# Kernel tuning notes

Hardware: AMD Instinct MI355X
Metric: run time of the kernel (lower is better)

## Reference

```python
import jax, jax.numpy as jnp
import numpy as np

# Module hyperparameters (from init_kwargs)
KH, KW = 3, 3          # kernel_size (must be 3x3: code hardcodes center tap 4 and 9 search positions)
SH, SW = 1, 1          # stride
PH, PW = 4, 4          # padding
DH, DW = 4, 4          # dilation
SD = DH // 2           # search_dilation


def setup_inputs() -> dict:
    key = jax.random.key(0)
    # positive depth values in meters-like range
    depth = jax.random.uniform(key, (4, 1, 480, 640), dtype=jnp.float32) * 10.0
    return {"depth": depth}


def _offset_search(depth):
    b, _, h, w = depth.shape
    outH = (h + 2 * PH - DH * (KH - 1) - 1) // SH + 1
    outW = (w + 2 * PW - DW * (KW - 1) - 1) // SW + 1
    d = depth[:, 0]  # [b, h, w]

    # --- first unfold: 3x3 window, dilation=SD, padding=SD, stride=1 ---
    # 9 zero-padded shifted copies of the depth map (the search samples)
    dp = jnp.pad(d, ((0, 0), (SD, SD), (SD, SD)))
    S = jnp.stack([dp[:, SD * r: SD * r + h, SD * c: SD * c + w]
                   for r in range(3) for c in range(3)], axis=1)  # [b, 9, h, w]

    # --- second unfold: kernel 3x3, dilation=(DH,DW), padding=(PH,PW), stride=(SH,SW) ---
    Sp = jnp.pad(S, ((0, 0), (0, 0), (PH, PH), (PW, PW)))
    rspan = SH * (outH - 1) + 1
    cspan = SW * (outW - 1) + 1
    taps = [Sp[:, :, DH * r: DH * r + rspan: SH, DW * c: DW * c + cspan: SW]
            for r in range(KH) for c in range(KW)]
    sample = jnp.stack(taps, axis=2)  # [b, 9(search), 9(kernel), outH, outW]

    # --- center tap (index 4) of unfold(depth) ---
    dpp = jnp.pad(d, ((0, 0), (PH, PH), (PW, PW)))
    center = dpp[:, DH: DH + rspan: SH, DW: DW + cspan: SW]  # [b, outH, outW]

    sample = jnp.abs(sample - center[:, None, None])

    # mask invalid search positions with +inf for border kernel taps 1,3,5,7
    inf = jnp.float32(jnp.inf)
    row_idx = jnp.array([0, 1, 2, 6, 7, 8])
    col_idx = jnp.array([0, 2, 3, 5, 6, 8])
    sample = sample.at[:, col_idx, 1].set(inf)
    sample = sample.at[:, row_idx, 3].set(inf)
    sample = sample.at[:, row_idx, 5].set(inf)
    sample = sample.at[:, col_idx, 7].set(inf)

    # argmin over the 9 search positions (first occurrence, like torch.min)
    idx = jnp.argmin(sample, axis=1)          # [b, 9, outH, outW]
    off_h = (idx // KH - 1) * SD
    off_w = (idx % KW - 1) * SD
    return jnp.concatenate([off_h, off_w], axis=1).astype(jnp.int32)  # [b, 18, outH, outW]


def reference(depth):
    return _offset_search(depth)
```

## Files before the change

kernel.cpp:

```cpp
#include <hip/hip_runtime.h>


#define BATCH 4
#define IH 480
#define IW 640

__global__ __launch_bounds__(256) void depth_offset_kernel(
    const float* __restrict__ d, int* __restrict__ out) {
  int idx = blockIdx.x * blockDim.x + threadIdx.x;
  if (idx >= BATCH * IH * IW) return;
  int ox = idx % IW;
  int t = idx / IW;
  int oy = t % IH;
  int b = t / IH;

  const float* __restrict__ db = d + (size_t)b * (IH * IW);
  float center = db[oy * IW + ox];

  float nb[7][7];
#pragma unroll
  for (int i = 0; i < 7; ++i) {
    int y = oy + 2 * i - 6;
    bool yok = ((unsigned)y < (unsigned)IH);
#pragma unroll
    for (int jj = 0; jj < 7; ++jj) {
      int x = ox + 2 * jj - 6;
      float v = 0.0f;
      if (yok && ((unsigned)x < (unsigned)IW)) v = db[y * IW + x];
      nb[i][jj] = v;
    }
  }

  const size_t plane = (size_t)IH * IW;
  int* __restrict__ outb = out + (size_t)b * 18 * plane;
  size_t pix = (size_t)oy * IW + ox;

#pragma unroll
  for (int j = 0; j < 9; ++j) {
    const int jr = j / 3, jc = j % 3;
    int Y = oy + 4 * (jr - 1);
    int X = ox + 4 * (jc - 1);
    bool jok = ((unsigned)Y < (unsigned)IH) && ((unsigned)X < (unsigned)IW);

    float best = __builtin_huge_valf();
    int bk = 0;
#pragma unroll
    for (int k = 0; k < 9; ++k) {
      const int kr = k / 3, kc = k % 3;
      bool allowed = true;
      if (j == 1 || j == 7) allowed = (kc == 1);
      if (j == 3 || j == 5) allowed = (kr == 1);
      if (!allowed) continue;

      float v = jok ? nb[2 * jr + kr][2 * jc + kc] : 0.0f;
      float diff = fabsf(v - center);
      if (diff < best) {
        best = diff;
        bk = k;
      }
    }
    outb[(size_t)j * plane + pix] = (bk / 3 - 1) * 2;
    outb[(size_t)(9 + j) * plane + pix] = (bk % 3 - 1) * 2;
  }
}

extern "C" void kernel_launch(void* const* d_in, const int* in_sizes, int n_in,
                              void* d_out, int out_size, void* d_ws, size_t ws_size,
                              hipStream_t stream) {
  const float* depth = (const float*)d_in[0];
  int* out = (int*)d_out;
  const int total = BATCH * IH * IW;
  const int block = 256;
  const int grid = (total + block - 1) / block;
  depth_offset_kernel<<<grid, block, 0, stream>>>(depth, out);
}
```

Baseline: 99.00 us.

## Pre-pad depth into workspace and process four pixels per thread with vector I/O

Result: slower. 102.3 us (+3.4%).

```diff
diff --git a/kernel.cpp b/kernel.cpp
--- a/kernel.cpp
+++ b/kernel.cpp
@@ -4,8 +4,174 @@
 #define BATCH 4
 #define IH 480
 #define IW 640
-
-__global__ __launch_bounds__(256) void depth_offset_kernel(
+#define PPW 656
+#define PPH 492
+#define PADBYTES ((size_t)BATCH * PPH * PPW * 4)
+
+__global__ __launch_bounds__(256) void pad_kernel(const float* __restrict__ d,
+                                                  float* __restrict__ pd) {
+  int idx = blockIdx.x * blockDim.x + threadIdx.x;
+  const int n4 = BATCH * PPH * (PPW / 4);
+  if (idx >= n4) return;
+  int c4 = idx % (PPW / 4);
+  int t = idx / (PPW / 4);
+  int r = t % PPH;
+  int b = t / PPH;
+  int y = r - 6;
+  float4 v = make_float4(0.f, 0.f, 0.f, 0.f);
+  if ((unsigned)y < (unsigned)IH) {
+    const float* src = d + ((size_t)b * IH + y) * IW;
+    int xb = c4 * 4 - 6;
+    float* vp = (float*)&v;
+#pragma unroll
+    for (int q = 0; q < 4; ++q) {
+      int x = xb + q;
+      if ((unsigned)x < (unsigned)IW) vp[q] = src[x];
+    }
+  }
+  ((float4*)pd)[idx] = v;
+}
+
+__global__ __launch_bounds__(256) void depth_offset_main(
+    const float* __restrict__ pd, int* __restrict__ out) {
+  const int NG = IW / 4;
+  int g = blockIdx.x * blockDim.x + threadIdx.x;
+  if (g >= BATCH * IH * NG) return;
+  int gx = g % NG;
+  int t = g / NG;
+  int oy = t % IH;
+  int b = t / IH;
+  int x0 = gx * 4;
+
+  const float* base = pd + ((size_t)b * PPH + oy) * PPW + x0;
+
+  float r0[16], r1[16], r2[16], r3[16], r4[16], r5[16], r6[16];
+#define LDROW(arr, i)                                              \
+  {                                                                \
+    const float4* rp = (const float4*)(base + (size_t)(2 * (i)) * PPW); \
+    *(float4*)&arr[0] = rp[0];                                     \
+    *(float4*)&arr[4] = rp[1];                                     \
+    *(float4*)&arr[8] = rp[2];                                     \
+    *(float4*)&arr[12] = rp[3];                                    \
+  }
+
+  const size_t plane = (size_t)IH * IW;
+  int* obase = out + (size_t)b * 18 * plane + (size_t)oy * IW + x0;
+#define STORE2(J, oh, ow)                                          \
+  {                                                                \
+    *(int4*)(obase + (size_t)(J)*plane) =                          \
+        make_int4(oh[0], oh[1], oh[2], oh[3]);                     \
+    *(int4*)(obase + (size_t)(9 + (J)) * plane) =                  \
+        make_int4(ow[0], ow[1], ow[2], ow[3]);                     \
+  }
+
+  bool yok0 = (oy >= 4), yok2 = (oy <= IH - 5);
+  bool xokL[4], xokR[4];
+#pragma unroll
+  for (int p = 0; p < 4; ++p) {
+    xokL[p] = (x0 + p >= 4);
+    xokR[p] = (x0 + p <= IW - 5);
+  }
+
+#define CAND(val, H, W)                  \
+  {                                      \
+    float df = fabsf((val)-cc);          \
+    if (df < best) {                     \
+      best = df;                         \
+      bh = (H);                          \
+      bw = (W);                          \
+    }                                    \
+  }
+
+#define DO_TAP9(J, RA, RB, RC, JC4, OKEXPR, FH, FW)                 \
+  {                                                                 \
+    int oh[4], ow[4];                                               \
+    _Pragma("unroll") for (int p = 0; p < 4; ++p) {                 \
+      float cc = cen[p];                                            \
+      int cb = p + (JC4);                                           \
+      float best = fabsf(RA[cb] - cc);                              \
+      int bh = -2, bw = -2;                                         \
+      CAND(RA[cb + 2], -2, 0)                                       \
+      CAND(RA[cb + 4], -2, 2)                                       \
+      CAND(RB[cb], 0, -2)                                           \
+      CAND(RB[cb + 2], 0, 0)                                        \
+      CAND(RB[cb + 4], 0, 2)                                        \
+      CAND(RC[cb], 2, -2)                                           \
+      CAND(RC[cb + 2], 2, 0)                                        \
+      CAND(RC[cb + 4], 2, 2)                                        \
+      bool ok = (OKEXPR);                                           \
+      oh[p] = ok ? bh : (FH);                                       \
+      ow[p] = ok ? bw : (FW);                                       \
+    }                                                               \
+    STORE2(J, oh, ow)                                               \
+  }
+
+#define DO_TAPV(J, RA, RB, RC, OKEXPR)                              \
+  {                                                                 \
+    int oh[4], ow[4];                                               \
+    _Pragma("unroll") for (int p = 0; p < 4; ++p) {                 \
+      float cc = cen[p];                                            \
+      int cb = p + 6;                                               \
+      float best = fabsf(RA[cb] - cc);                              \
+      int bh = -2;                                                  \
+      {                                                             \
+        float df = fabsf(RB[cb] - cc);                              \
+        if (df < best) { best = df; bh = 0; }                       \
+      }                                                             \
+      {                                                             \
+        float df = fabsf(RC[cb] - cc);                              \
+        if (df < best) { best = df; bh = 2; }                       \
+      }                                                             \
+      bool ok = (OKEXPR);                                           \
+      oh[p] = ok ? bh : -2;                                         \
+      ow[p] = 0;                                                    \
+    }                                                               \
+    STORE2(J, oh, ow)                                               \
+  }
+
+#define DO_TAPH(J, R, JC4, OKEXPR)                                  \
+  {                                                                 \
+    int oh[4], ow[4];                                               \
+    _Pragma("unroll") for (int p = 0; p < 4; ++p) {                 \
+      float cc = cen[p];                                            \
+      int cb = p + (JC4);                                           \
+      float best = fabsf(R[cb] - cc);                               \
+      int bw = -2;                                                  \
+      {                                                             \
+        float df = fabsf(R[cb + 2] - cc);                           \
+        if (df < best) { best = df; bw = 0; }                       \
+      }                                                             \
+      {                                                             \
+        float df = fabsf(R[cb + 4] - cc);                           \
+        if (df < best) { best = df; bw = 2; }                       \
+      }                                                             \
+      bool ok = (OKEXPR);                                           \
+      oh[p] = 0;                                                    \
+      ow[p] = ok ? bw : -2;                                         \
+    }                                                               \
+    STORE2(J, oh, ow)                                               \
+  }
+
+  LDROW(r0, 0)
+  LDROW(r1, 1)
+  LDROW(r2, 2)
+  LDROW(r3, 3)
+  float cen[4] = {r3[6], r3[7], r3[8], r3[9]};
+  LDROW(r4, 4)
+  DO_TAP9(0, r0, r1, r2, 0, yok0 && xokL[p], -2, -2)
+  DO_TAPV(1, r0, r1, r2, yok0)
+  DO_TAP9(2, r0, r1, r2, 8, yok0 && xokR[p], -2, -2)
+  LDROW(r5, 5)
+  LDROW(r6, 6)
+  DO_TAPH(3, r3, 0, xokL[p])
+  DO_TAP9(4, r2, r3, r4, 4, true, 0, 0)
+  DO_TAPH(5, r3, 8, xokR[p])
+  DO_TAP9(6, r4, r5, r6, 0, yok2 && xokL[p], -2, -2)
+  DO_TAPV(7, r4, r5, r6, yok2)
+  DO_TAP9(8, r4, r5, r6, 8, yok2 && xokR[p], -2, -2)
+}
+
+__global__ __launch_bounds__(256) void depth_offset_fallback(
     const float* __restrict__ d, int* __restrict__ out) {
   int idx = blockIdx.x * blockDim.x + threadIdx.x;
   if (idx >= BATCH * IH * IW) return;
@@ -13,10 +179,8 @@
   int t = idx / IW;
   int oy = t % IH;
   int b = t / IH;
-
-  const float* __restrict__ db = d + (size_t)b * (IH * IW);
+  const float* db = d + (size_t)b * (IH * IW);
   float center = db[oy * IW + ox];
-
   float nb[7][7];
 #pragma unroll
   for (int i = 0; i < 7; ++i) {
@@ -30,18 +194,15 @@
       nb[i][jj] = v;
     }
   }
-
   const size_t plane = (size_t)IH * IW;
-  int* __restrict__ outb = out + (size_t)b * 18 * plane;
+  int* outb = out + (size_t)b * 18 * plane;
   size_t pix = (size_t)oy * IW + ox;
-
 #pragma unroll
   for (int j = 0; j < 9; ++j) {
     const int jr = j / 3, jc = j % 3;
     int Y = oy + 4 * (jr - 1);
     int X = ox + 4 * (jc - 1);
     bool jok = ((unsigned)Y < (unsigned)IH) && ((unsigned)X < (unsigned)IW);
-
     float best = __builtin_huge_valf();
     int bk = 0;
 #pragma unroll
@@ -51,7 +212,6 @@
       if (j == 1 || j == 7) allowed = (kc == 1);
       if (j == 3 || j == 5) allowed = (kr == 1);
       if (!allowed) continue;
-
       float v = jok ? nb[2 * jr + kr][2 * jc + kc] : 0.0f;
       float diff = fabsf(v - center);
       if (diff < best) {
@@ -69,8 +229,14 @@
                               hipStream_t stream) {
   const float* depth = (const float*)d_in[0];
   int* out = (int*)d_out;
-  const int total = BATCH * IH * IW;
-  const int block = 256;
-  const int grid = (total + block - 1) / block;
-  depth_offset_kernel<<<grid, block, 0, stream>>>(depth, out);
-}
+  if (ws_size >= PADBYTES) {
+    float* pd = (float*)d_ws;
+    const int n4 = BATCH * PPH * (PPW / 4);
+    pad_kernel<<<(n4 + 255) / 256, 256, 0, stream>>>(depth, pd);
+    const int ngroups = BATCH * IH * (IW / 4);
+    depth_offset_main<<<(ngroups + 255) / 256, 256, 0, stream>>>(pd, out);
+  } else {
+    const int total = BATCH * IH * IW;
+    depth_offset_fallback<<<(total + 255) / 256, 256, 0, stream>>>(depth, out);
+  }
+}
```

## Tile depth into shared memory and compute four pixels per thread

Applied to the files above, without the earlier changes.

After: 104.7 us. 1.06x slower.

```diff
diff --git a/kernel.cpp b/kernel.cpp
--- a/kernel.cpp
+++ b/kernel.cpp
@@ -4,64 +4,192 @@
 #define BATCH 4
 #define IH 480
 #define IW 640
+#define TW 128
+#define TH 8
+#define LW 144
+#define LH 20
+#define NXT (IW / TW)
+#define NYT (IH / TH)
+
+typedef int iv4 __attribute__((ext_vector_type(4)));
 
 __global__ __launch_bounds__(256) void depth_offset_kernel(
     const float* __restrict__ d, int* __restrict__ out) {
-  int idx = blockIdx.x * blockDim.x + threadIdx.x;
-  if (idx >= BATCH * IH * IW) return;
-  int ox = idx % IW;
-  int t = idx / IW;
-  int oy = t % IH;
-  int b = t / IH;
+  __shared__ float T[LH * LW];
+
+  int blk = blockIdx.x;
+  int xt = blk % NXT;
+  int t = blk / NXT;
+  int yt = t % NYT;
+  int b = t / NYT;
+  int x0 = xt * TW;
+  int oy0 = yt * TH;
 
   const float* __restrict__ db = d + (size_t)b * (IH * IW);
-  float center = db[oy * IW + ox];
-
-  float nb[7][7];
+
+  bool interior = (xt > 0) && (xt < NXT - 1) && (yt > 0) && (yt < NYT - 1);
+  if (interior) {
+    const float* src = db + (size_t)(oy0 - 6) * IW + (x0 - 8);
 #pragma unroll
-  for (int i = 0; i < 7; ++i) {
-    int y = oy + 2 * i - 6;
-    bool yok = ((unsigned)y < (unsigned)IH);
-#pragma unroll
-    for (int jj = 0; jj < 7; ++jj) {
-      int x = ox + 2 * jj - 6;
-      float v = 0.0f;
-      if (yok && ((unsigned)x < (unsigned)IW)) v = db[y * IW + x];
-      nb[i][jj] = v;
-    }
-  }
-
-  const size_t plane = (size_t)IH * IW;
-  int* __restrict__ outb = out + (size_t)b * 18 * plane;
-  size_t pix = (size_t)oy * IW + ox;
-
-#pragma unroll
-  for (int j = 0; j < 9; ++j) {
-    const int jr = j / 3, jc = j % 3;
-    int Y = oy + 4 * (jr - 1);
-    int X = ox + 4 * (jc - 1);
-    bool jok = ((unsigned)Y < (unsigned)IH) && ((unsigned)X < (unsigned)IW);
-
-    float best = __builtin_huge_valf();
-    int bk = 0;
-#pragma unroll
-    for (int k = 0; k < 9; ++k) {
-      const int kr = k / 3, kc = k % 3;
-      bool allowed = true;
-      if (j == 1 || j == 7) allowed = (kc == 1);
-      if (j == 3 || j == 5) allowed = (kr == 1);
-      if (!allowed) continue;
-
-      float v = jok ? nb[2 * jr + kr][2 * jc + kc] : 0.0f;
-      float diff = fabsf(v - center);
-      if (diff < best) {
-        best = diff;
-        bk = k;
+    for (int it = 0; it < 3; ++it) {
+      int i = threadIdx.x + it * 256;
+      if (i < LH * (LW / 4)) {
+        int r = i / (LW / 4);
+        int c4 = i % (LW / 4);
+        *(float4*)&T[r * LW + c4 * 4] =
+            *(const float4*)(src + (size_t)r * IW + c4 * 4);
       }
     }
-    outb[(size_t)j * plane + pix] = (bk / 3 - 1) * 2;
-    outb[(size_t)(9 + j) * plane + pix] = (bk % 3 - 1) * 2;
-  }
+  } else {
+#pragma unroll
+    for (int it = 0; it < 12; ++it) {
+      int i = threadIdx.x + it * 256;
+      if (i < LH * LW) {
+        int r = i / LW;
+        int c = i % LW;
+        int y = oy0 + r - 6;
+        int x = x0 + c - 8;
+        float v = 0.0f;
+        if (((unsigned)y < (unsigned)IH) && ((unsigned)x < (unsigned)IW))
+          v = db[(size_t)y * IW + x];
+        T[r * LW + c] = v;
+      }
+    }
+  }
+  __syncthreads();
+
+  int gxi = threadIdx.x & 31;
+  int ry = threadIdx.x >> 5;
+  int px = x0 + gxi * 4;
+  int oy = oy0 + ry;
+
+  float R0[20], R1[20], R2[20];
+#define LDW(R, TROW)                                             \
+  {                                                              \
+    const float4* rp = (const float4*)&T[(TROW) * LW + gxi * 4]; \
+    *(float4*)&R[0] = rp[0];                                     \
+    *(float4*)&R[4] = rp[1];                                     \
+    *(float4*)&R[8] = rp[2];                                     \
+    *(float4*)&R[12] = rp[3];                                    \
+    *(float4*)&R[16] = rp[4];                                    \
+  }
+
+  float4 cen4 = *(const float4*)&T[(ry + 6) * LW + gxi * 4 + 8];
+  float cen[4] = {cen4.x, cen4.y, cen4.z, cen4.w};
+
+  const size_t plane = (size_t)IH * IW;
+  int* obase = out + (size_t)b * 18 * plane + (size_t)oy * IW + px;
+#define STORE2(J, oh, ow)                                              \
+  {                                                                    \
+    iv4 vh = {oh[0], oh[1], oh[2], oh[3]};                             \
+    iv4 vw = {ow[0], ow[1], ow[2], ow[3]};                             \
+    __builtin_nontemporal_store(vh, (iv4*)(obase + (size_t)(J)*plane)); \
+    __builtin_nontemporal_store(vw, (iv4*)(obase + (size_t)(9 + (J)) * plane)); \
+  }
+
+  bool yok0 = (oy >= 4), yok2 = (oy <= IH - 5);
+  bool xokL[4], xokR[4];
+#pragma unroll
+  for (int p = 0; p < 4; ++p) {
+    xokL[p] = (px + p >= 4);
+    xokR[p] = (px + p <= IW - 5);
+  }
+
+#define CAND(val, H, W)         \
+  {                             \
+    float df = fabsf((val)-cc); \
+    if (df < best) {            \
+      best = df;                \
+      bh = (H);                 \
+      bw = (W);                 \
+    }                           \
+  }
+
+#define DO_TAP9(J, RA, RB, RC, CB0, OKP, FH, FW)    \
+  {                                                 \
+    int oh[4], ow[4];                               \
+    _Pragma("unroll") for (int p = 0; p < 4; ++p) { \
+      float cc = cen[p];                            \
+      int cb = p + (CB0);                           \
+      float best = fabsf(RA[cb] - cc);              \
+      int bh = -2, bw = -2;                         \
+      CAND(RA[cb + 2], -2, 0)                       \
+      CAND(RA[cb + 4], -2, 2)                       \
+      CAND(RB[cb], 0, -2)                           \
+      CAND(RB[cb + 2], 0, 0)                        \
+      CAND(RB[cb + 4], 0, 2)                        \
+      CAND(RC[cb], 2, -2)                           \
+      CAND(RC[cb + 2], 2, 0)                        \
+      CAND(RC[cb + 4], 2, 2)                        \
+      bool ok = (OKP);                              \
+      oh[p] = ok ? bh : (FH);                       \
+      ow[p] = ok ? bw : (FW);                       \
+    }                                               \
+    STORE2(J, oh, ow)                               \
+  }
+
+#define DO_TAPV(J, RA, RB, RC, OKE)                 \
+  {                                                 \
+    int oh[4], ow[4];                               \
+    _Pragma("unroll") for (int p = 0; p < 4; ++p) { \
+      float cc = cen[p];                            \
+      int cb = p + 8;                               \
+      float best = fabsf(RA[cb] - cc);              \
+      int bh = -2;                                  \
+      {                                             \
+        float df = fabsf(RB[cb] - cc);              \
+        if (df < best) { best = df; bh = 0; }       \
+      }                                             \
+      {                                             \
+        float df = fabsf(RC[cb] - cc);              \
+        if (df < best) { best = df; bh = 2; }       \
+      }                                             \
+      bool ok = (OKE);                              \
+      oh[p] = ok ? bh : -2;                         \
+      ow[p] = 0;                                    \
+    }                                               \
+    STORE2(J, oh, ow)                               \
+  }
+
+#define DO_TAPH(J, R, CB0, OKP)                     \
+  {                                                 \
+    int oh[4], ow[4];                               \
+    _Pragma("unroll") for (int p = 0; p < 4; ++p) { \
+      float cc = cen[p];                            \
+      int cb = p + (CB0);                           \
+      float best = fabsf(R[cb] - cc);               \
+      int bw = -2;                                  \
+      {                                             \
+        float df = fabsf(R[cb + 2] - cc);           \
+        if (df < best) { best = df; bw = 0; }       \
+      }                                             \
+      {                                             \
+        float df = fabsf(R[cb + 4] - cc);           \
+        if (df < best) { best = df; bw = 2; }       \
+      }                                             \
+      bool ok = (OKP);                              \
+      oh[p] = 0;                                    \
+      ow[p] = ok ? bw : -2;                         \
+    }                                               \
+    STORE2(J, oh, ow)                               \
+  }
+
+  LDW(R0, ry)
+  LDW(R1, ry + 2)
+  LDW(R2, ry + 4)
+  DO_TAP9(0, R0, R1, R2, 2, yok0 && xokL[p], -2, -2)
+  DO_TAPV(1, R0, R1, R2, yok0)
+  DO_TAP9(2, R0, R1, R2, 10, yok0 && xokR[p], -2, -2)
+  LDW(R0, ry + 6)
+  LDW(R1, ry + 8)
+  DO_TAPH(3, R0, 2, xokL[p])
+  DO_TAP9(4, R2, R0, R1, 6, true, 0, 0)
+  DO_TAPH(5, R0, 10, xokR[p])
+  LDW(R2, ry + 10)
+  LDW(R0, ry + 12)
+  DO_TAP9(6, R1, R2, R0, 2, yok2 && xokL[p], -2, -2)
+  DO_TAPV(7, R1, R2, R0, yok2)
+  DO_TAP9(8, R1, R2, R0, 10, yok2 && xokR[p], -2, -2)
 }
 
 extern "C" void kernel_launch(void* const* d_in, const int* in_sizes, int n_in,
@@ -69,8 +197,6 @@
                               hipStream_t stream) {
   const float* depth = (const float*)d_in[0];
   int* out = (int*)d_out;
-  const int total = BATCH * IH * IW;
-  const int block = 256;
-  const int grid = (total + block - 1) / block;
-  depth_offset_kernel<<<grid, block, 0, stream>>>(depth, out);
+  const int nblocks = BATCH * NYT * NXT;
+  depth_offset_kernel<<<nblocks, 256, 0, stream>>>(depth, out);
 }
```

## Process four pixels per thread with vectorized row loads and nontemporal vector stores

Applied to the files above, without the earlier changes.

New measurement: 103.4 us. +4.5%, slower.

```diff
diff --git a/kernel.cpp b/kernel.cpp
--- a/kernel.cpp
+++ b/kernel.cpp
@@ -4,64 +4,173 @@
 #define BATCH 4
 #define IH 480
 #define IW 640
+#define NG (IW / 4)
+#define NPIX ((long)BATCH * IH * IW)
 
-__global__ __launch_bounds__(256) void depth_offset_kernel(
+typedef int iv4 __attribute__((ext_vector_type(4)));
+typedef float fv4 __attribute__((ext_vector_type(4)));
+
+__global__ __launch_bounds__(64) void depth_offset_kernel(
     const float* __restrict__ d, int* __restrict__ out) {
-  int idx = blockIdx.x * blockDim.x + threadIdx.x;
-  if (idx >= BATCH * IH * IW) return;
-  int ox = idx % IW;
-  int t = idx / IW;
+  int g = blockIdx.x * 64 + threadIdx.x;
+  int gx = g % NG;
+  int t = g / NG;
   int oy = t % IH;
   int b = t / IH;
+  int px = gx * 4;
 
   const float* __restrict__ db = d + (size_t)b * (IH * IW);
-  float center = db[oy * IW + ox];
 
-  float nb[7][7];
-#pragma unroll
-  for (int i = 0; i < 7; ++i) {
-    int y = oy + 2 * i - 6;
-    bool yok = ((unsigned)y < (unsigned)IH);
-#pragma unroll
-    for (int jj = 0; jj < 7; ++jj) {
-      int x = ox + 2 * jj - 6;
-      float v = 0.0f;
-      if (yok && ((unsigned)x < (unsigned)IW)) v = db[y * IW + x];
-      nb[i][jj] = v;
-    }
+  fv4 cen4 = *(const fv4*)(db + (size_t)oy * IW + px);
+  float cen[4] = {cen4.x, cen4.y, cen4.z, cen4.w};
+
+  bool xsafe = (px >= 8) && (px <= IW - 12);
+
+  float R0[20], R1[20], R2[20];
+#define LDG(R, i)                                                        \
+  {                                                                      \
+    int y = oy + 2 * (i) - 6;                                            \
+    if ((unsigned)y < (unsigned)IH) {                                    \
+      long a = ((long)(b * IH + y)) * IW + px - 8;                       \
+      if (xsafe || (a >= 0 && a + 20 <= NPIX)) {                         \
+        const fv4* rp = (const fv4*)(d + a);                             \
+        *(fv4*)&R[0] = rp[0];                                            \
+        *(fv4*)&R[4] = rp[1];                                            \
+        *(fv4*)&R[8] = rp[2];                                            \
+        *(fv4*)&R[12] = rp[3];                                           \
+        *(fv4*)&R[16] = rp[4];                                           \
+        if (!xsafe) {                                                    \
+          _Pragma("unroll") for (int c = 0; c < 20; ++c) {               \
+            int x = px + c - 8;                                          \
+            if ((unsigned)x >= (unsigned)IW) R[c] = 0.f;                 \
+          }                                                              \
+        }                                                                \
+      } else {                                                           \
+        const float* ry_ = db + (size_t)y * IW;                          \
+        _Pragma("unroll") for (int c = 0; c < 20; ++c) {                 \
+          int x = px + c - 8;                                            \
+          R[c] = ((unsigned)x < (unsigned)IW) ? ry_[x] : 0.f;            \
+        }                                                                \
+      }                                                                  \
+    } else {                                                             \
+      _Pragma("unroll") for (int c = 0; c < 20; ++c) R[c] = 0.f;         \
+    }                                                                    \
   }
 
   const size_t plane = (size_t)IH * IW;
-  int* __restrict__ outb = out + (size_t)b * 18 * plane;
-  size_t pix = (size_t)oy * IW + ox;
+  int* obase = out + (size_t)b * 18 * plane + (size_t)oy * IW + px;
+#define STORE2(J, oh, ow)                                               \
+  {                                                                     \
+    iv4 vh = {oh[0], oh[1], oh[2], oh[3]};                              \
+    iv4 vw = {ow[0], ow[1], ow[2], ow[3]};                              \
+    __builtin_nontemporal_store(vh, (iv4*)(obase + (size_t)(J)*plane)); \
+    __builtin_nontemporal_store(vw,                                     \
+                                (iv4*)(obase + (size_t)(9 + (J)) * plane)); \
+  }
 
+  bool yok0 = (oy >= 4), yok2 = (oy <= IH - 5);
+  bool okTL[4], okTR[4], okBL[4], okBR[4], xokL[4], xokR[4];
 #pragma unroll
-  for (int j = 0; j < 9; ++j) {
-    const int jr = j / 3, jc = j % 3;
-    int Y = oy + 4 * (jr - 1);
-    int X = ox + 4 * (jc - 1);
-    bool jok = ((unsigned)Y < (unsigned)IH) && ((unsigned)X < (unsigned)IW);
+  for (int p = 0; p < 4; ++p) {
+    xokL[p] = (px + p >= 4);
+    xokR[p] = (px + p <= IW - 5);
+    okTL[p] = yok0 && xokL[p];
+    okTR[p] = yok0 && xokR[p];
+    okBL[p] = yok2 && xokL[p];
+    okBR[p] = yok2 && xokR[p];
+  }
 
-    float best = __builtin_huge_valf();
-    int bk = 0;
-#pragma unroll
-    for (int k = 0; k < 9; ++k) {
-      const int kr = k / 3, kc = k % 3;
-      bool allowed = true;
-      if (j == 1 || j == 7) allowed = (kc == 1);
-      if (j == 3 || j == 5) allowed = (kr == 1);
-      if (!allowed) continue;
+#define DO_TAP9(J, RA, RB, RC, CB0, OKP)            \
+  {                                                 \
+    int oh[4], ow[4];                               \
+    _Pragma("unroll") for (int p = 0; p < 4; ++p) { \
+      float cc = cen[p];                            \
+      int cb = p + (CB0);                           \
+      float a0 = fabsf(RA[cb] - cc);                \
+      float a1 = fabsf(RA[cb + 2] - cc);            \
+      float a2 = fabsf(RA[cb + 4] - cc);            \
+      float a3 = fabsf(RB[cb] - cc);                \
+      float a4 = fabsf(RB[cb + 2] - cc);            \
+      float a5 = fabsf(RB[cb + 4] - cc);            \
+      float a6 = fabsf(RC[cb] - cc);                \
+      float a7 = fabsf(RC[cb + 2] - cc);            \
+      float a8 = fabsf(RC[cb + 4] - cc);            \
+      float m012 = fminf(fminf(a0, a1), a2);        \
+      float m345 = fminf(fminf(a3, a4), a5);        \
+      float m678 = fminf(fminf(a6, a7), a8);        \
+      float m = fminf(fminf(m012, m345), m678);     \
+      int code = 34;                                \
+      code = (a7 == m) ? 33 : code;                 \
+      code = (a6 == m) ? 32 : code;                 \
+      code = (a5 == m) ? 18 : code;                 \
+      code = (a4 == m) ? 17 : code;                 \
+      code = (a3 == m) ? 16 : code;                 \
+      code = (a2 == m) ? 2 : code;                  \
+      code = (a1 == m) ? 1 : code;                  \
+      code = (a0 == m) ? 0 : code;                  \
+      code = (OKP) ? code : 0;                      \
+      oh[p] = ((code >> 4) * 2) - 2;                \
+      ow[p] = ((code & 15) * 2) - 2;                \
+    }                                               \
+    STORE2(J, oh, ow)                               \
+  }
 
-      float v = jok ? nb[2 * jr + kr][2 * jc + kc] : 0.0f;
-      float diff = fabsf(v - center);
-      if (diff < best) {
-        best = diff;
-        bk = k;
-      }
-    }
-    outb[(size_t)j * plane + pix] = (bk / 3 - 1) * 2;
-    outb[(size_t)(9 + j) * plane + pix] = (bk % 3 - 1) * 2;
+#define DO_TAPV(J, RA, RB, RC, OKE)                 \
+  {                                                 \
+    int oh[4], ow[4];                               \
+    _Pragma("unroll") for (int p = 0; p < 4; ++p) { \
+      float cc = cen[p];                            \
+      int cb = p + 8;                                \
+      float a0 = fabsf(RA[cb] - cc);                \
+      float a1 = fabsf(RB[cb] - cc);                \
+      float a2 = fabsf(RC[cb] - cc);                \
+      float m = fminf(fminf(a0, a1), a2);           \
+      int code = 2;                                 \
+      code = (a1 == m) ? 1 : code;                  \
+      code = (a0 == m) ? 0 : code;                  \
+      code = (OKE) ? code : 0;                      \
+      oh[p] = code * 2 - 2;                         \
+      ow[p] = 0;                                    \
+    }                                               \
+    STORE2(J, oh, ow)                               \
   }
+
+#define DO_TAPH(J, R, CB0, OKP)                     \
+  {                                                 \
+    int oh[4], ow[4];                               \
+    _Pragma("unroll") for (int p = 0; p < 4; ++p) { \
+      float cc = cen[p];                            \
+      int cb = p + (CB0);                           \
+      float a0 = fabsf(R[cb] - cc);                 \
+      float a1 = fabsf(R[cb + 2] - cc);             \
+      float a2 = fabsf(R[cb + 4] - cc);             \
+      float m = fminf(fminf(a0, a1), a2);           \
+      int code = 2;                                 \
+      code = (a1 == m) ? 1 : code;                  \
+      code = (a0 == m) ? 0 : code;                  \
+      code = (OKP) ? code : 0;                      \
+      oh[p] = 0;                                    \
+      ow[p] = code * 2 - 2;                         \
+    }                                               \
+    STORE2(J, oh, ow)                               \
+  }
+
+  LDG(R0, 0)
+  LDG(R1, 1)
+  LDG(R2, 2)
+  DO_TAP9(0, R0, R1, R2, 2, okTL[p])
+  DO_TAPV(1, R0, R1, R2, yok0)
+  DO_TAP9(2, R0, R1, R2, 10, okTR[p])
+  LDG(R0, 3)
+  LDG(R1, 4)
+  DO_TAPH(3, R0, 2, xokL[p])
+  DO_TAP9(4, R2, R0, R1, 6, true)
+  DO_TAPH(5, R0, 10, xokR[p])
+  LDG(R2, 5)
+  LDG(R0, 6)
+  DO_TAP9(6, R1, R2, R0, 2, okBL[p])
+  DO_TAPV(7, R1, R2, R0, yok2)
+  DO_TAP9(8, R1, R2, R0, 10, okBR[p])
 }
 
 extern "C" void kernel_launch(void* const* d_in, const int* in_sizes, int n_in,
@@ -69,8 +178,6 @@
                               hipStream_t stream) {
   const float* depth = (const float*)d_in[0];
   int* out = (int*)d_out;
-  const int total = BATCH * IH * IW;
-  const int block = 256;
-  const int grid = (total + block - 1) / block;
-  depth_offset_kernel<<<grid, block, 0, stream>>>(depth, out);
+  const int nthreads = BATCH * IH * NG;
+  depth_offset_kernel<<<nthreads / 64, 64, 0, stream>>>(depth, out);
 }
```
